# Optimization experiments

Measured on AMD Instinct MI355X. Metric: run time of the kernel, lower is better.

Reference implementation:

```python
import jax, jax.numpy as jnp
import numpy as np

B, N, D = 8, 2048, 384

def setup_inputs() -> dict:
    key = jax.random.key(0)
    k1, k2, k3 = jax.random.split(key, 3)
    P_seq = jax.random.normal(k1, (B, N, D), dtype=jnp.float32)
    W = jax.random.normal(k2, (D, D), dtype=jnp.float32) / np.sqrt(D)
    b = jax.random.normal(k3, (1,), dtype=jnp.float32)
    return {"P_seq": P_seq, "W": W, "b": b}

def reference(P_seq, W, b):
    # nn.Bilinear(d, d, 1): logits[b,i,j] = P[b,i] @ W @ P[b,j] + bias
    # Efficient form: (P @ W) @ P^T, avoiding the O(B*N^2*D) expand.
    PW = jnp.einsum('bnd,de->bne', P_seq, W)          # [B, N, D]
    logits = jnp.einsum('bne,bme->bnm', PW, P_seq)    # [B, N, N]
    return logits + b[0]
```

## Files before the change

kernel.cpp:

```cpp
#include <hip/hip_runtime.h>
#include <stdint.h>


#define BATCH 8
#define NSEQ  2048
#define DDIM  384
#define BM 128
#define BN 128
#define BK 32

typedef __attribute__((ext_vector_type(8))) _Float16 half8;
typedef __attribute__((ext_vector_type(4))) _Float16 half4;
typedef __attribute__((ext_vector_type(4))) float    f32x4;

__global__ void cast_p_kernel(const float* __restrict__ in,
                              _Float16* __restrict__ out, int n) {
    int i = (blockIdx.x * blockDim.x + threadIdx.x) * 4;
    int stride = gridDim.x * blockDim.x * 4;
    for (; i < n; i += stride) {
        float4 f = *(const float4*)(in + i);
        half4 h;
        h.x = (_Float16)f.x; h.y = (_Float16)f.y;
        h.z = (_Float16)f.z; h.w = (_Float16)f.w;
        *(half4*)(out + i) = h;
    }
}

__global__ void transpose_w_kernel(const float* __restrict__ W,
                                   _Float16* __restrict__ Wt) {
    int o = blockIdx.x * blockDim.x + threadIdx.x;
    if (o < DDIM * DDIM) {
        int e = o / DDIM;
        int d = o - e * DDIM;
        Wt[o] = (_Float16)W[d * DDIM + e];
    }
}

template <bool OUT_HALF>
__global__ __launch_bounds__(256, 2) void gemm_bt_kernel(
    const _Float16* __restrict__ A,
    const _Float16* __restrict__ Bmat,
    void* __restrict__ Cv,
    const float* __restrict__ bias_ptr,
    long strideA, long strideB, long strideC, int ldc) {
    __shared__ _Float16 As[BM * BK];
    __shared__ _Float16 Bs[BN * BK];

    const _Float16* Ab = A + (size_t)blockIdx.z * strideA
                           + (size_t)blockIdx.y * BM * DDIM;
    const _Float16* Bb = Bmat + (size_t)blockIdx.z * strideB
                              + (size_t)blockIdx.x * BN * DDIM;

    const int tid  = threadIdx.x;
    const int wave = tid >> 6;
    const int lane = tid & 63;
    const int wrow = wave >> 1;
    const int wcol = wave & 1;
    const int lcol = lane & 15;
    const int kq   = lane >> 4;

    f32x4 acc[4][4];
#pragma unroll
    for (int i = 0; i < 4; ++i)
#pragma unroll
        for (int j = 0; j < 4; ++j)
            acc[i][j] = (f32x4){0.f, 0.f, 0.f, 0.f};

    for (int k0 = 0; k0 < DDIM; k0 += BK) {
#pragma unroll
        for (int p = 0; p < 2; ++p) {
            int c  = p * 256 + tid;
            int r  = c >> 2;
            int kc = (c & 3) * 8;
            __builtin_amdgcn_global_load_lds(
                (const __attribute__((address_space(1))) void*)
                    (Ab + (size_t)r * DDIM + k0 + kc),
                (__attribute__((address_space(3))) void*)(As + c * 8),
                16, 0, 0);
            __builtin_amdgcn_global_load_lds(
                (const __attribute__((address_space(1))) void*)
                    (Bb + (size_t)r * DDIM + k0 + kc),
                (__attribute__((address_space(3))) void*)(Bs + c * 8),
                16, 0, 0);
        }
        __syncthreads();

        half8 af[4], bf[4];
#pragma unroll
        for (int t = 0; t < 4; ++t) {
            int m = wrow * 64 + t * 16 + lcol;
            af[t] = *(const half8*)(As + m * BK + kq * 8);
            int n = wcol * 64 + t * 16 + lcol;
            bf[t] = *(const half8*)(Bs + n * BK + kq * 8);
        }
#pragma unroll
        for (int i = 0; i < 4; ++i)
#pragma unroll
            for (int j = 0; j < 4; ++j)
                acc[i][j] = __builtin_amdgcn_mfma_f32_16x16x32_f16(
                    af[i], bf[j], acc[i][j], 0, 0, 0);
        __syncthreads();
    }

    const size_t row0 = (size_t)blockIdx.y * BM + wrow * 64 + kq * 4;
    const size_t col0 = (size_t)blockIdx.x * BN + wcol * 64 + lcol;
    if (OUT_HALF) {
        _Float16* Cb = (_Float16*)Cv + (size_t)blockIdx.z * strideC;
#pragma unroll
        for (int i = 0; i < 4; ++i)
#pragma unroll
            for (int j = 0; j < 4; ++j)
#pragma unroll
                for (int r = 0; r < 4; ++r)
                    Cb[(row0 + i * 16 + r) * ldc + col0 + j * 16] =
                        (_Float16)acc[i][j][r];
    } else {
        const float bias = bias_ptr[0];
        float* Cb = (float*)Cv + (size_t)blockIdx.z * strideC;
#pragma unroll
        for (int i = 0; i < 4; ++i)
#pragma unroll
            for (int j = 0; j < 4; ++j)
#pragma unroll
                for (int r = 0; r < 4; ++r)
                    Cb[(row0 + i * 16 + r) * ldc + col0 + j * 16] =
                        acc[i][j][r] + bias;
    }
}

extern "C" void kernel_launch(void* const* d_in, const int* in_sizes, int n_in,
                              void* d_out, int out_size, void* d_ws,
                              size_t ws_size, hipStream_t stream) {
    const float* P  = (const float*)d_in[0];
    const float* W  = (const float*)d_in[1];
    const float* bp = (const float*)d_in[2];
    float* out = (float*)d_out;

    _Float16* Ph = (_Float16*)d_ws;
    _Float16* Wt = Ph + (size_t)BATCH * NSEQ * DDIM;
    _Float16* PW = Wt + (size_t)DDIM * DDIM;

    const int nP = BATCH * NSEQ * DDIM;
    cast_p_kernel<<<1024, 256, 0, stream>>>(P, Ph, nP);
    transpose_w_kernel<<<(DDIM * DDIM + 255) / 256, 256, 0, stream>>>(W, Wt);

    dim3 g1(DDIM / BN, (BATCH * NSEQ) / BM, 1);
    gemm_bt_kernel<true><<<g1, 256, 0, stream>>>(
        Ph, Wt, (void*)PW, nullptr, 0L, 0L, 0L, DDIM);

    dim3 g2(NSEQ / BN, NSEQ / BM, BATCH);
    gemm_bt_kernel<false><<<g2, 256, 0, stream>>>(
        PW, Ph, (void*)out, bp,
        (long)NSEQ * DDIM, (long)NSEQ * DDIM, (long)NSEQ * NSEQ, NSEQ);
}
```

Before: 199.2 us.

## Switch GEMM to 32x32x16 MFMA with BK=64 and XOR-swizzled LDS layout

Replaces the 16x16x32 MFMA tiling with 32x32x16 MFMA instructions (2x2 per wave), doubles the K tile to 64, and applies an XOR swizzle on LDS chunk placement to avoid bank conflicts on fragment reads. This halves the number of K-loop iterations and barriers and reduces LDS read traffic per MFMA. The output mapping is rewritten for the 32x32 accumulator layout, which makes stores less contiguous per row, and LDS use doubles, which could affect occupancy.

```diff
diff --git a/kernel.cpp b/kernel.cpp
--- a/kernel.cpp
+++ b/kernel.cpp
@@ -7,11 +7,11 @@
 #define DDIM  384
 #define BM 128
 #define BN 128
-#define BK 32
+#define BK 64
 
-typedef __attribute__((ext_vector_type(8))) _Float16 half8;
-typedef __attribute__((ext_vector_type(4))) _Float16 half4;
-typedef __attribute__((ext_vector_type(4))) float    f32x4;
+typedef __attribute__((ext_vector_type(8)))  _Float16 half8;
+typedef __attribute__((ext_vector_type(4)))  _Float16 half4;
+typedef __attribute__((ext_vector_type(16))) float    f32x16;
 
 __global__ void cast_p_kernel(const float* __restrict__ in,
                               _Float16* __restrict__ out, int n) {
@@ -56,75 +56,90 @@
     const int lane = tid & 63;
     const int wrow = wave >> 1;
     const int wcol = wave & 1;
-    const int lcol = lane & 15;
-    const int kq   = lane >> 4;
+    const int lm   = lane & 31;
+    const int hi   = lane >> 5;
 
-    f32x4 acc[4][4];
+    const int srow = tid >> 3;
+    const int scg  = ((tid & 7) ^ (srow & 7)) * 8;
+
+    const int h0     = (hi ^ (lm & 7)) * 16;
+    const int baseA0 = (wrow * 64 + lm) * (BK * 2) + h0;
+    const int baseA1 = baseA0 + 32 * (BK * 2);
+    const int baseB0 = (wcol * 64 + lm) * (BK * 2) + h0;
+    const int baseB1 = baseB0 + 32 * (BK * 2);
+    const char* AsB = (const char*)As;
+    const char* BsB = (const char*)Bs;
+
+    f32x16 acc[2][2];
 #pragma unroll
-    for (int i = 0; i < 4; ++i)
+    for (int i = 0; i < 2; ++i)
 #pragma unroll
-        for (int j = 0; j < 4; ++j)
-            acc[i][j] = (f32x4){0.f, 0.f, 0.f, 0.f};
+        for (int j = 0; j < 2; ++j)
+#pragma unroll
+            for (int r = 0; r < 16; ++r)
+                acc[i][j][r] = 0.f;
 
     for (int k0 = 0; k0 < DDIM; k0 += BK) {
 #pragma unroll
-        for (int p = 0; p < 2; ++p) {
-            int c  = p * 256 + tid;
-            int r  = c >> 2;
-            int kc = (c & 3) * 8;
+        for (int p = 0; p < 4; ++p) {
+            const int r = p * 32 + srow;
             __builtin_amdgcn_global_load_lds(
                 (const __attribute__((address_space(1))) void*)
-                    (Ab + (size_t)r * DDIM + k0 + kc),
-                (__attribute__((address_space(3))) void*)(As + c * 8),
+                    (Ab + (size_t)r * DDIM + k0 + scg),
+                (__attribute__((address_space(3))) void*)
+                    (As + (p * 256 + tid) * 8),
                 16, 0, 0);
             __builtin_amdgcn_global_load_lds(
                 (const __attribute__((address_space(1))) void*)
-                    (Bb + (size_t)r * DDIM + k0 + kc),
-                (__attribute__((address_space(3))) void*)(Bs + c * 8),
+                    (Bb + (size_t)r * DDIM + k0 + scg),
+                (__attribute__((address_space(3))) void*)
+                    (Bs + (p * 256 + tid) * 8),
                 16, 0, 0);
         }
         __syncthreads();
 
-        half8 af[4], bf[4];
 #pragma unroll
-        for (int t = 0; t < 4; ++t) {
-            int m = wrow * 64 + t * 16 + lcol;
-            af[t] = *(const half8*)(As + m * BK + kq * 8);
-            int n = wcol * 64 + t * 16 + lcol;
-            bf[t] = *(const half8*)(Bs + n * BK + kq * 8);
+        for (int s = 0; s < 4; ++s) {
+            const int sx = s * 32;
+            half8 a0 = *(const half8*)(AsB + (baseA0 ^ sx));
+            half8 a1 = *(const half8*)(AsB + (baseA1 ^ sx));
+            half8 b0 = *(const half8*)(BsB + (baseB0 ^ sx));
+            half8 b1 = *(const half8*)(BsB + (baseB1 ^ sx));
+            acc[0][0] = __builtin_amdgcn_mfma_f32_32x32x16_f16(a0, b0, acc[0][0], 0, 0, 0);
+            acc[0][1] = __builtin_amdgcn_mfma_f32_32x32x16_f16(a0, b1, acc[0][1], 0, 0, 0);
+            acc[1][0] = __builtin_amdgcn_mfma_f32_32x32x16_f16(a1, b0, acc[1][0], 0, 0, 0);
+            acc[1][1] = __builtin_amdgcn_mfma_f32_32x32x16_f16(a1, b1, acc[1][1], 0, 0, 0);
         }
-#pragma unroll
-        for (int i = 0; i < 4; ++i)
-#pragma unroll
-            for (int j = 0; j < 4; ++j)
-                acc[i][j] = __builtin_amdgcn_mfma_f32_16x16x32_f16(
-                    af[i], bf[j], acc[i][j], 0, 0, 0);
         __syncthreads();
     }
 
-    const size_t row0 = (size_t)blockIdx.y * BM + wrow * 64 + kq * 4;
-    const size_t col0 = (size_t)blockIdx.x * BN + wcol * 64 + lcol;
+    const size_t row_base = (size_t)blockIdx.y * BM + wrow * 64;
+    const size_t col_base = (size_t)blockIdx.x * BN + wcol * 64;
     if (OUT_HALF) {
         _Float16* Cb = (_Float16*)Cv + (size_t)blockIdx.z * strideC;
 #pragma unroll
-        for (int i = 0; i < 4; ++i)
+        for (int i = 0; i < 2; ++i)
 #pragma unroll
-            for (int j = 0; j < 4; ++j)
+            for (int j = 0; j < 2; ++j)
 #pragma unroll
-                for (int r = 0; r < 4; ++r)
-                    Cb[(row0 + i * 16 + r) * ldc + col0 + j * 16] =
-                        (_Float16)acc[i][j][r];
+                for (int reg = 0; reg < 16; ++reg) {
+                    const int rin = (reg & 3) + 8 * (reg >> 2) + 4 * hi;
+                    Cb[(row_base + i * 32 + rin) * ldc
+                       + col_base + j * 32 + lm] = (_Float16)acc[i][j][reg];
+                }
     } else {
         const float bias = bias_ptr[0];
         float* Cb = (float*)Cv + (size_t)blockIdx.z * strideC;
 #pragma unroll
-        for (int i = 0; i < 4; ++i)
+        for (int i = 0; i < 2; ++i)
 #pragma unroll
-            for (int j = 0; j < 4; ++j)
+            for (int j = 0; j < 2; ++j)
 #pragma unroll
-                for (int r = 0; r < 4; ++r)
-                    Cb[(row0 + i * 16 + r) * ldc + col0 + j * 16] =
-                        acc[i][j][r] + bias;
+                for (int reg = 0; reg < 16; ++reg) {
+                    const int rin = (reg & 3) + 8 * (reg >> 2) + 4 * hi;
+                    Cb[(row_base + i * 32 + rin) * ldc
+                       + col_base + j * 32 + lm] = acc[i][j][reg] + bias;
+                }
     }
 }
 
```

Result: faster. 190.8 us (-4.2%).
